# Kernel optimization log

Measured on AMD Instinct MI355X. Metric: run time of the kernel, lower is better.

## Reference

```python
import jax, jax.numpy as jnp
import numpy as np

H = 1024; B = 8; L = 4096
DI = 2048   # d_inner = expand*H
DS = 16     # d_state
DC = 4      # d_conv
DR = 64     # dt_rank = ceil(H/16)
HR = 256    # H // 4 hourglass


def setup_inputs() -> dict:
    key = jax.random.key(0)
    ks = jax.random.split(key, 16)
    w = lambda k, s, sc=0.02: jax.random.normal(k, s, jnp.float32) * sc
    return {
        "x": jax.random.normal(ks[0], (B, L, H), jnp.float32),
        "c": jax.random.normal(ks[1], (B, H), jnp.float32),
        "adaln_w": w(ks[2], (3 * H, H)), "adaln_b": jnp.zeros((3 * H,), jnp.float32),
        "hgd_w1": w(ks[3], (HR, H)), "hgd_b1": jnp.zeros((HR,), jnp.float32),
        "hgd_w2": w(ks[4], (H, HR)), "hgd_b2": jnp.zeros((H,), jnp.float32),
        "hgf_wm": w(ks[5], (HR, H)), "hgf_bm": jnp.zeros((HR,), jnp.float32),
        "hgf_wr": w(ks[6], (HR, H)), "hgf_br": jnp.zeros((HR,), jnp.float32),
        "hgf_wf": w(ks[7], (H, HR)), "hgf_bf": jnp.zeros((H,), jnp.float32),
        "in_w": w(ks[8], (2 * DI, H)),
        "conv_w": w(ks[9], (DI, DC), 0.1), "conv_b": jnp.zeros((DI,), jnp.float32),
        "xproj_w": w(ks[10], (DR + 2 * DS, DI)),
        "dtproj_w": w(ks[11], (DI, DR), 0.1),
        "dt_bias": jnp.full((DI,), -4.6, jnp.float32),  # softplus -> dt ~ 0.01
        "A_log": jnp.log(jnp.tile(jnp.arange(1, DS + 1, dtype=jnp.float32), (DI, 1))),
        "D": jnp.ones((DI,), jnp.float32),
        "out_w": w(ks[12], (H, DI)),
    }


def reference(x, c, adaln_w, adaln_b, hgd_w1, hgd_b1, hgd_w2, hgd_b2,
              hgf_wm, hgf_bm, hgf_wr, hgf_br, hgf_wf, hgf_bf,
              in_w, conv_w, conv_b, xproj_w, dtproj_w, dt_bias, A_log, D, out_w):
    silu = jax.nn.silu
    # adaLN-Zero conditioning: SiLU -> Linear -> 3 chunks
    mod = silu(c) @ adaln_w.T + adaln_b                      # [B, 3H]
    shift, scale, alpha = jnp.split(mod, 3, axis=1)          # each [B, H]
    # LayerNorm (no affine, eps=1e-6)
    mu = x.mean(-1, keepdims=True)
    var = x.var(-1, keepdims=True)
    xn = (x - mu) / jnp.sqrt(var + 1e-6)
    x1 = xn * (1.0 + scale[:, None, :]) + shift[:, None, :]  # modulate
    # Hourglass dense: Linear(H->H/4) -> SiLU -> Linear(H/4->H)
    hd = silu(x1 @ hgd_w1.T + hgd_b1) @ hgd_w2.T + hgd_b2    # [B, L, H]
    # ---- Mamba ----
    xz = hd @ in_w.T                                         # [B, L, 2*DI]
    xm, z = jnp.split(xz, 2, axis=-1)
    # causal depthwise conv1d
    xc = jnp.transpose(xm, (0, 2, 1))                        # [B, DI, L]
    xc = jax.lax.conv_general_dilated(
        xc, conv_w[:, None, :], (1,), [(DC - 1, 0)],
        feature_group_count=DI, dimension_numbers=("NCH", "OIH", "NCH"))
    xc = silu(xc + conv_b[None, :, None])
    xc = jnp.transpose(xc, (0, 2, 1))                        # [B, L, DI]
    # input-dependent dt, B, C
    dbl = xc @ xproj_w.T                                     # [B, L, DR+2*DS]
    dt, Bm, Cm = jnp.split(dbl, [DR, DR + DS], axis=-1)
    dt = jax.nn.softplus(dt @ dtproj_w.T + dt_bias)          # [B, L, DI]
    A = -jnp.exp(A_log)                                      # [DI, DS]
    # selective scan: h_{t} = exp(dt*A)*h_{t-1} + dt*B_t*x_t ; y_t = <h_t, C_t>
    def step(h, inp):
        dt_t, B_t, C_t, x_t = inp                            # [B,DI],[B,DS],[B,DS],[B,DI]
        h = h * jnp.exp(dt_t[:, :, None] * A) + (dt_t * x_t)[:, :, None] * B_t[:, None, :]
        return h, jnp.einsum("bds,bs->bd", h, C_t)
    h0 = jnp.zeros((x.shape[0], DI, DS), x.dtype)
    seq = (jnp.transpose(dt, (1, 0, 2)), jnp.transpose(Bm, (1, 0, 2)),
           jnp.transpose(Cm, (1, 0, 2)), jnp.transpose(xc, (1, 0, 2)))
    _, ys = jax.lax.scan(step, h0, seq)                      # [L, B, DI]
    y = jnp.transpose(ys, (1, 0, 2)) + xc * D
    y = y * silu(z)
    x1_2 = y @ out_w.T                                       # [B, L, H]
    # Hourglass fusion
    fused = (silu(x1_2 @ hgf_wm.T + hgf_bm) * silu(x1 @ hgf_wr.T + hgf_br)) @ hgf_wf.T + hgf_bf
    return x + alpha[:, None, :] * fused
```

## Files before the change

kernel.cpp:

```cpp
#include <hip/hip_runtime.h>

#define Hn 1024
#define Bn 8
#define Ln 4096
#define DIn 2048
#define NCH 64
#define CLn 64

typedef __attribute__((ext_vector_type(8))) short short8;
typedef __attribute__((ext_vector_type(4))) short short4v;
typedef __attribute__((ext_vector_type(4))) float f32x4;

__device__ __forceinline__ float bf2f(short s) {
  return __uint_as_float(((unsigned)(unsigned short)s) << 16);
}
__device__ __forceinline__ short f2bf(float f) {
  unsigned u = __float_as_uint(f);
  u += 0x7fffu + ((u >> 16) & 1u);
  return (short)(u >> 16);
}
__device__ __forceinline__ float silu_f(float x) { return x / (1.f + __expf(-x)); }
__device__ __forceinline__ float softplus_f(float x) { return x > 20.f ? x : log1pf(__expf(x)); }

__device__ __forceinline__ void gld16(const short* g, short* l) {
  __builtin_amdgcn_global_load_lds((const __attribute__((address_space(1))) void*)g,
                                   (__attribute__((address_space(3))) void*)l, 16, 0, 0);
}

__global__ __launch_bounds__(256) void f2bf4_kernel(const float* __restrict__ in,
                                                    short* __restrict__ out, int n4) {
  int i = blockIdx.x * 256 + threadIdx.x;
  if (i < n4) {
    f32x4 v = ((const f32x4*)in)[i];
    short4v o;
    o.x = f2bf(v.x); o.y = f2bf(v.y); o.z = f2bf(v.z); o.w = f2bf(v.w);
    ((short4v*)out)[i] = o;
  }
}

__global__ __launch_bounds__(256) void modcalc_kernel(const float* __restrict__ c,
    const float* __restrict__ aw, const float* __restrict__ ab, float* __restrict__ mod) {
  int wid = blockIdx.x * 4 + (threadIdx.x >> 6);
  int lane = threadIdx.x & 63;
  int b = wid / 3072, n = wid - b * 3072;
  const f32x4* cr = (const f32x4*)(c + b * Hn);
  const f32x4* wr = (const f32x4*)(aw + (size_t)n * Hn);
  float s = 0.f;
#pragma unroll
  for (int i = 0; i < 4; ++i) {
    f32x4 cv = cr[lane + 64 * i];
    f32x4 wv = wr[lane + 64 * i];
    s += silu_f(cv.x) * wv.x + silu_f(cv.y) * wv.y + silu_f(cv.z) * wv.z + silu_f(cv.w) * wv.w;
  }
#pragma unroll
  for (int m = 1; m < 64; m <<= 1) s += __shfl_xor(s, m, 64);
  if (lane == 0) mod[wid] = s + ab[n];
}

__global__ __launch_bounds__(256) void ln_mod_kernel(const float* __restrict__ x,
    const float* __restrict__ mod, short* __restrict__ x1, int b0) {
  int row = blockIdx.x * 4 + (threadIdx.x >> 6);
  int lane = threadIdx.x & 63;
  int b = b0 + (row >> 12);
  const f32x4* xr = (const f32x4*)(x + (size_t)row * Hn);
  f32x4 v[4];
  float s = 0.f, ss = 0.f;
#pragma unroll
  for (int i = 0; i < 4; ++i) {
    v[i] = xr[lane + 64 * i];
    s += v[i].x + v[i].y + v[i].z + v[i].w;
    ss += v[i].x * v[i].x + v[i].y * v[i].y + v[i].z * v[i].z + v[i].w * v[i].w;
  }
#pragma unroll
  for (int m = 1; m < 64; m <<= 1) {
    s += __shfl_xor(s, m, 64);
    ss += __shfl_xor(ss, m, 64);
  }
  float mu = s * (1.f / 1024.f);
  float var = ss * (1.f / 1024.f) - mu * mu;
  float r = rsqrtf(var + 1e-6f);
  const f32x4* shp = (const f32x4*)(mod + b * 3072);
  const f32x4* scp = (const f32x4*)(mod + b * 3072 + 1024);
#pragma unroll
  for (int i = 0; i < 4; ++i) {
    int k4 = lane + 64 * i;
    f32x4 sc = scp[k4], sh = shp[k4];
    short4v o;
    o.x = f2bf((v[i].x - mu) * r * (1.f + sc.x) + sh.x);
    o.y = f2bf((v[i].y - mu) * r * (1.f + sc.y) + sh.y);
    o.z = f2bf((v[i].z - mu) * r * (1.f + sc.z) + sh.z);
    o.w = f2bf((v[i].w - mu) * r * (1.f + sc.w) + sh.w);
    *(short4v*)&x1[(size_t)row * Hn + k4 * 4] = o;
  }
}

#define SA_STR 40
template <int EPI>
__global__ __launch_bounds__(256) void gemm_k(
    const short* __restrict__ A, const short* __restrict__ W,
    const float* __restrict__ bias, const short* mul,
    const float* __restrict__ xres, const float* __restrict__ modp,
    void* outp, int N, int K, int b0) {
  __shared__ short sA[2][128 * SA_STR];
  __shared__ short sB[2][128 * SA_STR];
  int tid = threadIdx.x;
  int wave = tid >> 6, lane = tid & 63;
  int bm0 = blockIdx.y * 128;
  int bn0 = blockIdx.x * 128;
  int wm = (wave >> 1) * 64, wn = (wave & 1) * 64;
  int lrow = lane & 15, kh = (lane >> 4) * 8;
  int srow = tid >> 2;
  int scol = (tid & 3) * 8;

  f32x4 acc[4][4];
#pragma unroll
  for (int i = 0; i < 4; i++)
#pragma unroll
    for (int j = 0; j < 4; j++) acc[i][j] = (f32x4)0.f;

#pragma unroll
  for (int p = 0; p < 2; ++p) {
    int r = srow + p * 64;
    short8 av = *(const short8*)&A[(size_t)(bm0 + r) * K + scol];
    *(short8*)&sA[0][r * SA_STR + scol] = av;
    int n = bn0 + r;
    short8 bv = (short8)0;
    if (n < N) bv = *(const short8*)&W[(size_t)n * K + scol];
    *(short8*)&sB[0][r * SA_STR + scol] = bv;
  }
  __syncthreads();

  int cur = 0;
  for (int k0 = 0; k0 < K; k0 += 32) {
    bool have = (k0 + 32) < K;
    short8 av[2], bv[2];
    if (have) {
#pragma unroll
      for (int p = 0; p < 2; ++p) {
        int r = srow + p * 64;
        av[p] = *(const short8*)&A[(size_t)(bm0 + r) * K + k0 + 32 + scol];
        int n = bn0 + r;
        bv[p] = (short8)0;
        if (n < N) bv[p] = *(const short8*)&W[(size_t)n * K + k0 + 32 + scol];
      }
    }
    short8 af[4], bfr[4];
#pragma unroll
    for (int i = 0; i < 4; i++) af[i] = *(const short8*)&sA[cur][(wm + i * 16 + lrow) * SA_STR + kh];
#pragma unroll
    for (int j = 0; j < 4; j++) bfr[j] = *(const short8*)&sB[cur][(wn + j * 16 + lrow) * SA_STR + kh];
#pragma unroll
    for (int i = 0; i < 4; i++)
#pragma unroll
      for (int j = 0; j < 4; j++)
        acc[i][j] = __builtin_amdgcn_mfma_f32_16x16x32_bf16(af[i], bfr[j], acc[i][j], 0, 0, 0);
    if (have) {
      int nxt = cur ^ 1;
#pragma unroll
      for (int p = 0; p < 2; ++p) {
        int r = srow + p * 64;
        *(short8*)&sA[nxt][r * SA_STR + scol] = av[p];
        *(short8*)&sB[nxt][r * SA_STR + scol] = bv[p];
      }
    }
    __syncthreads();
    cur ^= 1;
  }

  int orow4 = (lane >> 4) * 4;
  int ocol = lane & 15;
#pragma unroll
  for (int i = 0; i < 4; i++)
#pragma unroll
    for (int j = 0; j < 4; j++)
#pragma unroll
      for (int r = 0; r < 4; r++) {
        int row = bm0 + wm + i * 16 + orow4 + r;
        int col = bn0 + wn + j * 16 + ocol;
        if (col >= N) continue;
        float v = acc[i][j][r];
        size_t idx = (size_t)row * N + col;
        if (EPI == 0) {
          ((short*)outp)[idx] = f2bf(v);
        } else if (EPI == 1) {
          ((short*)outp)[idx] = f2bf(v + bias[col]);
        } else if (EPI == 2) {
          ((short*)outp)[idx] = f2bf(silu_f(v + bias[col]));
        } else if (EPI == 3) {
          ((short*)outp)[idx] = f2bf(softplus_f(v + bias[col]));
        } else if (EPI == 4) {
          float t = silu_f(v + bias[col]) * bf2f(mul[idx]);
          ((short*)outp)[idx] = f2bf(t);
        } else if (EPI == 5) {
          ((float*)outp)[idx] = v;
        } else if (EPI == 6) {
          int b = b0 + (row >> 12);
          float t = v + bias[col];
          ((float*)outp)[idx] = xres[idx] + modp[b * 3072 + 2048 + col] * t;
        } else if (EPI == 7) {
          float t = silu_f(v) * bf2f(mul[idx]);
          ((short*)outp)[idx] = f2bf(t);
        } else if (EPI == 8) {
          ((float*)outp)[idx] = v;
          if (col < 64) ((short*)mul)[(size_t)row * 64 + col] = f2bf(v);
        }
      }
}

template <int EPI>
__global__ __launch_bounds__(512, 1) void gemm256_k(
    const short* __restrict__ A, const short* __restrict__ W,
    const short* mul, void* outp, int N, int K) {
  __shared__ short sA[2][256 * 64];
  __shared__ short sB[2][256 * 64];
  int tid = threadIdx.x;
  int wave = tid >> 6, lane = tid & 63;
  int nwg = gridDim.x * gridDim.y;
  int orig = blockIdx.y * gridDim.x + blockIdx.x;
  int cpx = nwg >> 3;
  int wg = (orig & 7) * cpx + (orig >> 3);
  int bm0 = (wg / gridDim.x) * 256;
  int bn0 = (wg % gridDim.x) * 256;
  int wm = (wave >> 2) * 128, wn = (wave & 3) * 64;
  int lrow = lane & 15;
  int kq = (lane >> 4) * 8;
  int srow = tid >> 3;
  int scol = (tid & 7) * 8;
  int soff = srow * 64 + scol;

  const short* Ab = A + (size_t)(bm0 + srow) * K + scol;
  const short* Bb = W + (size_t)(bn0 + srow) * K + scol;

  f32x4 acc[8][4];
#pragma unroll
  for (int m = 0; m < 8; m++)
#pragma unroll
    for (int n = 0; n < 4; n++) acc[m][n] = (f32x4)0.f;

#pragma unroll
  for (int p = 0; p < 4; ++p) {
    gld16(Ab + (size_t)(64 * p) * K, &sA[0][soff + p * 64 * 64]);
    gld16(Bb + (size_t)(64 * p) * K, &sB[0][soff + p * 64 * 64]);
  }
  __syncthreads();

  int cur = 0;
  for (int k0 = 0; k0 < K; k0 += 64) {
    int nxt = cur ^ 1;
    if (k0 + 64 < K) {
#pragma unroll
      for (int p = 0; p < 4; ++p) {
        gld16(Ab + k0 + 64 + (size_t)(64 * p) * K, &sA[nxt][soff + p * 64 * 64]);
        gld16(Bb + k0 + 64 + (size_t)(64 * p) * K, &sB[nxt][soff + p * 64 * 64]);
      }
    }
#pragma unroll
    for (int ks = 0; ks < 2; ++ks) {
      short8 af[8], bfr[4];
#pragma unroll
      for (int m = 0; m < 8; ++m)
        af[m] = *(const short8*)&sA[cur][(wm + m * 16 + lrow) * 64 + ks * 32 + kq];
#pragma unroll
      for (int n = 0; n < 4; ++n)
        bfr[n] = *(const short8*)&sB[cur][(wn + n * 16 + lrow) * 64 + ks * 32 + kq];
#pragma unroll
      for (int m = 0; m < 8; ++m)
#pragma unroll
        for (int n = 0; n < 4; ++n)
          acc[m][n] = __builtin_amdgcn_mfma_f32_16x16x32_bf16(af[m], bfr[n], acc[m][n], 0, 0, 0);
    }
    __syncthreads();
    cur = nxt;
  }

  int orow4 = (lane >> 4) * 4;
  int ocol = lane & 15;
#pragma unroll
  for (int m = 0; m < 8; m++)
#pragma unroll
    for (int n = 0; n < 4; n++)
#pragma unroll
      for (int r = 0; r < 4; r++) {
        int row = bm0 + wm + m * 16 + orow4 + r;
        int col = bn0 + wn + n * 16 + ocol;
        float v = acc[m][n][r];
        size_t idx = (size_t)row * N + col;
        if (EPI == 0) {
          ((short*)outp)[idx] = f2bf(v);
        } else if (EPI == 7) {
          float t = silu_f(v) * bf2f(mul[idx]);
          ((short*)outp)[idx] = f2bf(t);
        }
      }
}

__global__ __launch_bounds__(256) void conv_kernel(const short* __restrict__ xm,
    const float* __restrict__ cw, const float* __restrict__ cb, short* __restrict__ xc) {
  size_t idx = (size_t)blockIdx.x * 256 + threadIdx.x;
  int d = (int)(idx & (DIn - 1));
  size_t bt = idx >> 11;
  int t = (int)(bt & (Ln - 1));
  f32x4 w = *(const f32x4*)(cw + d * 4);
  float wj[4] = {w.x, w.y, w.z, w.w};
  float acc = cb[d];
#pragma unroll
  for (int j = 0; j < 4; ++j) {
    int tt = t - 3 + j;
    if (tt >= 0) acc += bf2f(xm[(bt - 3 + j) * DIn + d]) * wj[j];
  }
  xc[idx] = f2bf(silu_f(acc));
}

__global__ __launch_bounds__(256) void scan_part1(const short* __restrict__ dt,
    const short* __restrict__ xc, const float* __restrict__ dbl,
    const float* __restrict__ A_log, float* __restrict__ hq, float* __restrict__ sd) {
  __shared__ float sB[CLn * 16];
  int tid = threadIdx.x;
  int g = blockIdx.x * 256 + tid;
  int d = g & (DIn - 1);
  int r = g >> 11;
  int c = r & (NCH - 1);
  int b = r >> 6;
  size_t rb = (size_t)b * Ln + (size_t)c * CLn;
  {
    int row = tid >> 2, q = tid & 3;
    *(f32x4*)&sB[row * 16 + q * 4] = *(const f32x4*)(dbl + (rb + row) * 96 + 64 + q * 4);
  }
  __syncthreads();
  float A[16], h[16];
#pragma unroll
  for (int s = 0; s < 16; ++s) {
    A[s] = -__expf(A_log[d * 16 + s]);
    h[s] = 0.f;
  }
  bool st = true;
#pragma unroll
  for (int s = 1; s < 16; ++s)
    st = st && (fabsf(A[s] - (float)(s + 1) * A[0]) <= 1e-4f * fabsf(A[s]));
  float A0 = A[0];
  float sum = 0.f;
  const short* dp = dt + rb * DIn + d;
  const short* xp = xc + rb * DIn + d;
  short dtn = *dp, xcn = *xp;
  if (st) {
    for (int t = 0; t < CLn; ++t) {
      float dtv = bf2f(dtn), xv = bf2f(xcn);
      int tn = (t + 1 < CLn) ? t + 1 : t;
      dtn = dp[(size_t)tn * DIn];
      xcn = xp[(size_t)tn * DIn];
      float u = dtv * xv;
      sum += dtv;
      const f32x4* bp = (const f32x4*)&sB[t * 16];
      f32x4 b0 = bp[0], b1 = bp[1], b2 = bp[2], b3 = bp[3];
      float bv[16] = {b0.x, b0.y, b0.z, b0.w, b1.x, b1.y, b1.z, b1.w,
                      b2.x, b2.y, b2.z, b2.w, b3.x, b3.y, b3.z, b3.w};
      float qe = __expf(dtv * A0);
      float pk = qe;
#pragma unroll
      for (int s = 0; s < 16; ++s) {
        h[s] = h[s] * pk + u * bv[s];
        pk *= qe;
      }
    }
  } else {
    for (int t = 0; t < CLn; ++t) {
      float dtv = bf2f(dtn), xv = bf2f(xcn);
      int tn = (t + 1 < CLn) ? t + 1 : t;
      dtn = dp[(size_t)tn * DIn];
      xcn = xp[(size_t)tn * DIn];
      float u = dtv * xv;
      sum += dtv;
      const f32x4* bp = (const f32x4*)&sB[t * 16];
      f32x4 b0 = bp[0], b1 = bp[1], b2 = bp[2], b3 = bp[3];
      float bv[16] = {b0.x, b0.y, b0.z, b0.w, b1.x, b1.y, b1.z, b1.w,
                      b2.x, b2.y, b2.z, b2.w, b3.x, b3.y, b3.z, b3.w};
#pragma unroll
      for (int s = 0; s < 16; ++s) h[s] = h[s] * __expf(dtv * A[s]) + u * bv[s];
    }
  }
  size_t bd = (size_t)b * DIn + d;
  f32x4* out = (f32x4*)(hq + (bd * NCH + c) * 16);
#pragma unroll
  for (int i = 0; i < 4; ++i) {
    f32x4 o; o.x = h[4 * i]; o.y = h[4 * i + 1]; o.z = h[4 * i + 2]; o.w = h[4 * i + 3];
    out[i] = o;
  }
  sd[bd * NCH + c] = sum;
}

__global__ __launch_bounds__(256) void scan_combine(const float* __restrict__ A_log,
    const float* __restrict__ sd, float* hq) {
  int g = blockIdx.x * 256 + threadIdx.x;
  int s = g & 15;
  size_t bd = (size_t)(g >> 4);
  int d = (int)(bd & (DIn - 1));
  float A = -__expf(A_log[d * 16 + s]);
  float H = 0.f;
  for (int c = 0; c < NCH; ++c) {
    size_t idx = (bd * NCH + c) * 16 + s;
    float he = hq[idx];
    float e = __expf(A * sd[bd * NCH + c]);
    hq[idx] = H;
    H = H * e + he;
  }
}

__global__ __launch_bounds__(256) void scan_part2(const short* dt,
    const short* __restrict__ xc, const float* __restrict__ dbl,
    const float* __restrict__ A_log, const float* __restrict__ Dv,
    const float* __restrict__ hq, short* y) {
  __shared__ float sBC[CLn * 32];
  int tid = threadIdx.x;
  int g = blockIdx.x * 256 + tid;
  int d = g & (DIn - 1);
  int r = g >> 11;
  int c = r & (NCH - 1);
  int b = r >> 6;
  size_t rb = (size_t)b * Ln + (size_t)c * CLn;
  {
    int row = tid >> 2, q = tid & 3;
    const float* src = dbl + (rb + row) * 96 + 64 + q * 8;
    *(f32x4*)&sBC[row * 32 + q * 8] = *(const f32x4*)src;
    *(f32x4*)&sBC[row * 32 + q * 8 + 4] = *(const f32x4*)(src + 4);
  }
  __syncthreads();
  size_t bd = (size_t)b * DIn + d;
  float A[16], h[16];
#pragma unroll
  for (int s = 0; s < 16; ++s) A[s] = -__expf(A_log[d * 16 + s]);
  const f32x4* hin = (const f32x4*)(hq + (bd * NCH + c) * 16);
#pragma unroll
  for (int i = 0; i < 4; ++i) {
    f32x4 qv = hin[i];
    h[4 * i] = qv.x; h[4 * i + 1] = qv.y; h[4 * i + 2] = qv.z; h[4 * i + 3] = qv.w;
  }
  bool st = true;
#pragma unroll
  for (int s = 1; s < 16; ++s)
    st = st && (fabsf(A[s] - (float)(s + 1) * A[0]) <= 1e-4f * fabsf(A[s]));
  float A0 = A[0];
  float Dd = Dv[d];
  const short* dp = dt + rb * DIn + d;
  const short* xp = xc + rb * DIn + d;
  short* yp = y + rb * DIn + d;
  short dtn = *dp, xcn = *xp;
  if (st) {
    for (int t = 0; t < CLn; ++t) {
      float dtv = bf2f(dtn), xv = bf2f(xcn);
      int tn = (t + 1 < CLn) ? t + 1 : t;
      dtn = dp[(size_t)tn * DIn];
      xcn = xp[(size_t)tn * DIn];
      float u = dtv * xv;
      const f32x4* pp = (const f32x4*)&sBC[t * 32];
      f32x4 v0 = pp[0], v1 = pp[1], v2 = pp[2], v3 = pp[3];
      f32x4 v4 = pp[4], v5 = pp[5], v6 = pp[6], v7 = pp[7];
      float bc[32] = {v0.x, v0.y, v0.z, v0.w, v1.x, v1.y, v1.z, v1.w,
                      v2.x, v2.y, v2.z, v2.w, v3.x, v3.y, v3.z, v3.w,
                      v4.x, v4.y, v4.z, v4.w, v5.x, v5.y, v5.z, v5.w,
                      v6.x, v6.y, v6.z, v6.w, v7.x, v7.y, v7.z, v7.w};
      float qe = __expf(dtv * A0);
      float pk = qe, acc = 0.f;
#pragma unroll
      for (int s = 0; s < 16; ++s) {
        h[s] = h[s] * pk + u * bc[s];
        acc += h[s] * bc[16 + s];
        pk *= qe;
      }
      yp[(size_t)t * DIn] = f2bf(acc + xv * Dd);
    }
  } else {
    for (int t = 0; t < CLn; ++t) {
      float dtv = bf2f(dtn), xv = bf2f(xcn);
      int tn = (t + 1 < CLn) ? t + 1 : t;
      dtn = dp[(size_t)tn * DIn];
      xcn = xp[(size_t)tn * DIn];
      float u = dtv * xv;
      const f32x4* pp = (const f32x4*)&sBC[t * 32];
      f32x4 v0 = pp[0], v1 = pp[1], v2 = pp[2], v3 = pp[3];
      f32x4 v4 = pp[4], v5 = pp[5], v6 = pp[6], v7 = pp[7];
      float bc[32] = {v0.x, v0.y, v0.z, v0.w, v1.x, v1.y, v1.z, v1.w,
                      v2.x, v2.y, v2.z, v2.w, v3.x, v3.y, v3.z, v3.w,
                      v4.x, v4.y, v4.z, v4.w, v5.x, v5.y, v5.z, v5.w,
                      v6.x, v6.y, v6.z, v6.w, v7.x, v7.y, v7.z, v7.w};
      float acc = 0.f;
#pragma unroll
      for (int s = 0; s < 16; ++s) {
        h[s] = h[s] * __expf(dtv * A[s]) + u * bc[s];
        acc += h[s] * bc[16 + s];
      }
      yp[(size_t)t * DIn] = f2bf(acc + xv * Dd);
    }
  }
}

extern "C" void kernel_launch(void* const* d_in, const int* in_sizes, int n_in,
                              void* d_out, int out_size, void* d_ws, size_t ws_size,
                              hipStream_t stream) {
  const float* x = (const float*)d_in[0];
  const float* c = (const float*)d_in[1];
  const float* adaln_w = (const float*)d_in[2];
  const float* adaln_b = (const float*)d_in[3];
  const float* hgd_w1 = (const float*)d_in[4];
  const float* hgd_b1 = (const float*)d_in[5];
  const float* hgd_w2 = (const float*)d_in[6];
  const float* hgd_b2 = (const float*)d_in[7];
  const float* hgf_wm = (const float*)d_in[8];
  const float* hgf_bm = (const float*)d_in[9];
  const float* hgf_wr = (const float*)d_in[10];
  const float* hgf_br = (const float*)d_in[11];
  const float* hgf_wf = (const float*)d_in[12];
  const float* hgf_bf = (const float*)d_in[13];
  const float* in_w = (const float*)d_in[14];
  const float* conv_w = (const float*)d_in[15];
  const float* conv_b = (const float*)d_in[16];
  const float* xproj_w = (const float*)d_in[17];
  const float* dtproj_w = (const float*)d_in[18];
  const float* dt_bias = (const float*)d_in[19];
  const float* A_log = (const float*)d_in[20];
  const float* Dv = (const float*)d_in[21];
  const float* out_w = (const float*)d_in[22];
  (void)in_sizes; (void)n_in; (void)out_size;

  char* ws = (char*)d_ws;
  size_t off = 0;
  auto alloc = [&](size_t bytes) -> void* {
    void* p = ws + off;
    off += (bytes + 255) & ~(size_t)255;
    return p;
  };
  short* w1b = (short*)alloc((size_t)256 * 1024 * 2);
  short* w2b = (short*)alloc((size_t)1024 * 256 * 2);
  short* wmb = (short*)alloc((size_t)256 * 1024 * 2);
  short* wrb = (short*)alloc((size_t)256 * 1024 * 2);
  short* wfb = (short*)alloc((size_t)1024 * 256 * 2);
  short* inwb = (short*)alloc((size_t)4096 * 1024 * 2);
  short* xpb = (short*)alloc((size_t)96 * 2048 * 2);
  short* dtpb = (short*)alloc((size_t)2048 * 64 * 2);
  short* owb = (short*)alloc((size_t)1024 * 2048 * 2);
  float* modb = (float*)alloc((size_t)Bn * 3072 * 4);
  size_t persist = off;

  int BC = 8;
  while (BC > 1 && persist + (size_t)BC * Ln * 14976 > ws_size) BC >>= 1;
  int nchunk = 8 / BC;
  size_t Mc = (size_t)BC * Ln;

  short* x1 = (short*)alloc(Mc * 1024 * 2);
  short* hd = (short*)alloc(Mc * 1024 * 2);
  short* xm = (short*)alloc(Mc * 2048 * 2);
  short* xct = (short*)alloc(Mc * 2048 * 2);
  float* dbl = (float*)alloc(Mc * 96 * 4);
  short* dtb = (short*)alloc(Mc * 64 * 2);
  float* hq = (float*)alloc((size_t)BC * DIn * NCH * 16 * 4);
  float* sd = (float*)alloc((size_t)BC * DIn * NCH * 4);
  short* t1 = xct;

  auto conv1 = [&](const float* src, short* dst, int n) {
    f2bf4_kernel<<<(n / 4 + 255) / 256, 256, 0, stream>>>(src, dst, n / 4);
  };
  conv1(hgd_w1, w1b, 256 * 1024);
  conv1(hgd_w2, w2b, 1024 * 256);
  conv1(hgf_wm, wmb, 256 * 1024);
  conv1(hgf_wr, wrb, 256 * 1024);
  conv1(hgf_wf, wfb, 1024 * 256);
  conv1(in_w, inwb, 4096 * 1024);
  conv1(xproj_w, xpb, 96 * 2048);
  conv1(dtproj_w, dtpb, 2048 * 64);
  conv1(out_w, owb, 1024 * 2048);

  modcalc_kernel<<<(Bn * 3072) / 4, 256, 0, stream>>>(c, adaln_w, adaln_b, modb);

  dim3 blk(256);
  dim3 blk512(512);
  int gy = (int)(Mc / 128);
  int gy256 = (int)(Mc / 256);
  for (int ck = 0; ck < nchunk; ++ck) {
    int b0 = ck * BC;
    const float* xch = x + (size_t)b0 * Ln * Hn;
    float* och = (float*)d_out + (size_t)b0 * Ln * Hn;

    ln_mod_kernel<<<(int)(Mc / 4), blk, 0, stream>>>(xch, modb, x1, b0);
    gemm_k<2><<<dim3(2, gy), blk, 0, stream>>>(x1, w1b, hgd_b1, nullptr, nullptr, nullptr, t1, 256, 1024, 0);
    gemm_k<1><<<dim3(8, gy), blk, 0, stream>>>(t1, w2b, hgd_b2, nullptr, nullptr, nullptr, hd, 1024, 256, 0);
    gemm256_k<0><<<dim3(8, gy256), blk512, 0, stream>>>(hd, inwb, nullptr, xm, 2048, 1024);
    conv_kernel<<<(int)(Mc * 2048 / 256), blk, 0, stream>>>(xm, conv_w, conv_b, xct);
    gemm_k<8><<<dim3(1, gy), blk, 0, stream>>>(xct, xpb, nullptr, dtb, nullptr, nullptr, dbl, 96, 2048, 0);
    gemm_k<3><<<dim3(16, gy), blk, 0, stream>>>(dtb, dtpb, dt_bias, nullptr, nullptr, nullptr, xm, 2048, 64, 0);
    scan_part1<<<(int)(BC * 512), blk, 0, stream>>>(xm, xct, dbl, A_log, hq, sd);
    scan_combine<<<(int)(BC * 128), blk, 0, stream>>>(A_log, sd, hq);
    scan_part2<<<(int)(BC * 512), blk, 0, stream>>>(xm, xct, dbl, A_log, Dv, hq, xm);
    gemm256_k<7><<<dim3(8, gy256), blk512, 0, stream>>>(hd, inwb + (size_t)2048 * 1024, xm, xm, 2048, 1024);
    gemm256_k<0><<<dim3(4, gy256), blk512, 0, stream>>>(xm, owb, nullptr, hd, 1024, 2048);
    gemm_k<2><<<dim3(2, gy), blk, 0, stream>>>(hd, wmb, hgf_bm, nullptr, nullptr, nullptr, t1, 256, 1024, 0);
    gemm_k<4><<<dim3(2, gy), blk, 0, stream>>>(x1, wrb, hgf_br, t1, nullptr, nullptr, t1, 256, 1024, 0);
    gemm_k<6><<<dim3(8, gy), blk, 0, stream>>>(t1, wfb, hgf_bf, nullptr, xch, modb, och, 1024, 256, b0);
  }
}
```

Measured before the change: 2.091 ms.

## Rewrite 256x256 GEMM as 8-phase pipelined kernel with swizzled LDS

Replaces the simple double-buffered 256x256 bf16 GEMM with an 8-phase schedule. Each K-tile pair is split into quarter MFMA blocks, and half-tile global-to-LDS loads are interleaved between them, separated by explicit barriers and sched_barrier fences. LDS uses an XOR-swizzled layout to avoid bank conflicts, and MFMA blocks run at raised wave priority. The aim is to hide global load latency and LDS read stalls behind matrix math, at the cost of many more barriers and hand-tuned vmcnt waits that depend on K being a multiple of 128.

Measured after the change: 2.102 ms. No clear change (+0.5%).

```diff
diff --git a/kernel.cpp b/kernel.cpp
--- a/kernel.cpp
+++ b/kernel.cpp
@@ -26,6 +26,14 @@
   __builtin_amdgcn_global_load_lds((const __attribute__((address_space(1))) void*)g,
                                    (__attribute__((address_space(3))) void*)l, 16, 0, 0);
 }
+
+#define PFENCE() __builtin_amdgcn_sched_barrier(0)
+#define PBAR()            \
+  do {                    \
+    PFENCE();             \
+    __builtin_amdgcn_s_barrier(); \
+    PFENCE();             \
+  } while (0)
 
 __global__ __launch_bounds__(256) void f2bf4_kernel(const float* __restrict__ in,
                                                     short* __restrict__ out, int n4) {
@@ -208,11 +216,11 @@
 }
 
 template <int EPI>
-__global__ __launch_bounds__(512, 1) void gemm256_k(
+__global__ __launch_bounds__(512, 1) void gemm256_8ph(
     const short* __restrict__ A, const short* __restrict__ W,
     const short* mul, void* outp, int N, int K) {
-  __shared__ short sA[2][256 * 64];
-  __shared__ short sB[2][256 * 64];
+  __shared__ short sMem[65536];
+  char* sRaw = (char*)sMem;
   int tid = threadIdx.x;
   int wave = tid >> 6, lane = tid & 63;
   int nwg = gridDim.x * gridDim.y;
@@ -221,58 +229,132 @@
   int wg = (orig & 7) * cpx + (orig >> 3);
   int bm0 = (wg / gridDim.x) * 256;
   int bn0 = (wg % gridDim.x) * 256;
+  int lrow = lane & 15;
+  int lnOff = lrow * 64 + (((lane >> 4) * 16) ^ ((lrow >> 3) << 5));
+  int aBase = (wave >> 2) * 16384 + lnOff;
+  int bBase = 32768 + ((wave & 3) >> 1) * 16384 + lnOff;
+  int bSub = (wave & 1) * 4;
+
+  int rS[2], cS[2], lSlot[2];
+#pragma unroll
+  for (int p = 0; p < 2; ++p) {
+    int s = p * 8 + wave;
+    rS[p] = (s >> 1) * 16 + (lane >> 2);
+    cS[p] = (s & 1) * 4 + ((lane & 3) ^ (((lane >> 5) & 1) << 1));
+    lSlot[p] = s * 1024 + lane * 16;
+  }
+
+  f32x4 acc[8][4];
+#pragma unroll
+  for (int m = 0; m < 8; m++)
+#pragma unroll
+    for (int n = 0; n < 4; n++) acc[m][n] = (f32x4)0.f;
+
+  auto stage = [&](const short* Mb, int row0, int tt, int hh, int isB) {
+    int rb = (tt & 1) * 65536 + isB * 32768 + hh * 16384;
+#pragma unroll
+    for (int p = 0; p < 2; ++p) {
+      const short* src = Mb + (size_t)(row0 + hh * 128 + rS[p]) * K + tt * 64 + cS[p] * 8;
+      gld16(src, (short*)(sRaw + rb + lSlot[p]));
+    }
+  };
+
+  short8 af[4][2], bfL[2][2], bfH[2][2];
+  auto loadA = [&](int mg, int bsel) {
+#pragma unroll
+    for (int m = 0; m < 4; ++m)
+#pragma unroll
+      for (int ks = 0; ks < 2; ++ks)
+        af[m][ks] =
+            *(const short8*)(sRaw + bsel * 65536 + aBase + ((mg * 4 + m) * 2 + ks) * 1024);
+  };
+  auto loadB = [&](short8(&bf)[2][2], int ng, int bsel) {
+#pragma unroll
+    for (int n = 0; n < 2; ++n)
+#pragma unroll
+      for (int ks = 0; ks < 2; ++ks)
+        bf[n][ks] = *(const short8*)(sRaw + bsel * 65536 + bBase +
+                                     ((bSub + ng * 2 + n) * 2 + ks) * 1024);
+  };
+  auto mmaQ = [&](short8(&bf)[2][2], int mg, int ng) {
+    __builtin_amdgcn_s_setprio(1);
+#pragma unroll
+    for (int ks = 0; ks < 2; ++ks)
+#pragma unroll
+      for (int m = 0; m < 4; ++m)
+#pragma unroll
+        for (int n = 0; n < 2; ++n)
+          acc[mg * 4 + m][ng * 2 + n] = __builtin_amdgcn_mfma_f32_16x16x32_bf16(
+              af[m][ks], bf[n][ks], acc[mg * 4 + m][ng * 2 + n], 0, 0, 0);
+    __builtin_amdgcn_s_setprio(0);
+  };
+
+  stage(A, bm0, 0, 0, 0);
+  stage(A, bm0, 0, 1, 0);
+  stage(W, bn0, 0, 0, 1);
+  stage(W, bn0, 0, 1, 1);
+  stage(W, bn0, 1, 0, 1);
+  stage(W, bn0, 1, 1, 1);
+  asm volatile("s_waitcnt vmcnt(4)" ::: "memory");
+  PBAR();
+
+  int NT = K >> 6;
+  for (int t = 0; t < NT; t += 2) {
+    int s2 = (t + 2) < NT, s3 = (t + 3) < NT;
+    loadA(0, 0);
+    loadB(bfL, 0, 0);
+    stage(A, bm0, t + 1, 0, 0);
+    PBAR();
+    mmaQ(bfL, 0, 0);
+    PBAR();
+    loadB(bfH, 1, 0);
+    stage(A, bm0, t + 1, 1, 0);
+    PBAR();
+    mmaQ(bfH, 0, 1);
+    PBAR();
+    loadA(1, 0);
+    if (s2) stage(W, bn0, t + 2, 0, 1);
+    PBAR();
+    mmaQ(bfL, 1, 0);
+    PBAR();
+    if (s2) {
+      stage(W, bn0, t + 2, 1, 1);
+      asm volatile("s_waitcnt vmcnt(4)" ::: "memory");
+    } else {
+      asm volatile("s_waitcnt vmcnt(0)" ::: "memory");
+    }
+    PBAR();
+    mmaQ(bfH, 1, 1);
+    PBAR();
+    loadA(0, 1);
+    loadB(bfL, 0, 1);
+    if (s2) stage(A, bm0, t + 2, 0, 0);
+    PBAR();
+    mmaQ(bfL, 0, 0);
+    PBAR();
+    loadB(bfH, 1, 1);
+    if (s2) stage(A, bm0, t + 2, 1, 0);
+    PBAR();
+    mmaQ(bfH, 0, 1);
+    PBAR();
+    loadA(1, 1);
+    if (s3) stage(W, bn0, t + 3, 0, 1);
+    PBAR();
+    mmaQ(bfL, 1, 0);
+    PBAR();
+    if (s3) stage(W, bn0, t + 3, 1, 1);
+    if (s2) {
+      if (s3)
+        asm volatile("s_waitcnt vmcnt(4)" ::: "memory");
+      else
+        asm volatile("s_waitcnt vmcnt(0)" ::: "memory");
+    }
+    PBAR();
+    mmaQ(bfH, 1, 1);
+    PBAR();
+  }
+
   int wm = (wave >> 2) * 128, wn = (wave & 3) * 64;
-  int lrow = lane & 15;
-  int kq = (lane >> 4) * 8;
-  int srow = tid >> 3;
-  int scol = (tid & 7) * 8;
-  int soff = srow * 64 + scol;
-
-  const short* Ab = A + (size_t)(bm0 + srow) * K + scol;
-  const short* Bb = W + (size_t)(bn0 + srow) * K + scol;
-
-  f32x4 acc[8][4];
-#pragma unroll
-  for (int m = 0; m < 8; m++)
-#pragma unroll
-    for (int n = 0; n < 4; n++) acc[m][n] = (f32x4)0.f;
-
-#pragma unroll
-  for (int p = 0; p < 4; ++p) {
-    gld16(Ab + (size_t)(64 * p) * K, &sA[0][soff + p * 64 * 64]);
-    gld16(Bb + (size_t)(64 * p) * K, &sB[0][soff + p * 64 * 64]);
-  }
-  __syncthreads();
-
-  int cur = 0;
-  for (int k0 = 0; k0 < K; k0 += 64) {
-    int nxt = cur ^ 1;
-    if (k0 + 64 < K) {
-#pragma unroll
-      for (int p = 0; p < 4; ++p) {
-        gld16(Ab + k0 + 64 + (size_t)(64 * p) * K, &sA[nxt][soff + p * 64 * 64]);
-        gld16(Bb + k0 + 64 + (size_t)(64 * p) * K, &sB[nxt][soff + p * 64 * 64]);
-      }
-    }
-#pragma unroll
-    for (int ks = 0; ks < 2; ++ks) {
-      short8 af[8], bfr[4];
-#pragma unroll
-      for (int m = 0; m < 8; ++m)
-        af[m] = *(const short8*)&sA[cur][(wm + m * 16 + lrow) * 64 + ks * 32 + kq];
-#pragma unroll
-      for (int n = 0; n < 4; ++n)
-        bfr[n] = *(const short8*)&sB[cur][(wn + n * 16 + lrow) * 64 + ks * 32 + kq];
-#pragma unroll
-      for (int m = 0; m < 8; ++m)
-#pragma unroll
-        for (int n = 0; n < 4; ++n)
-          acc[m][n] = __builtin_amdgcn_mfma_f32_16x16x32_bf16(af[m], bfr[n], acc[m][n], 0, 0, 0);
-    }
-    __syncthreads();
-    cur = nxt;
-  }
-
   int orow4 = (lane >> 4) * 4;
   int ocol = lane & 15;
 #pragma unroll
@@ -582,15 +664,15 @@
     ln_mod_kernel<<<(int)(Mc / 4), blk, 0, stream>>>(xch, modb, x1, b0);
     gemm_k<2><<<dim3(2, gy), blk, 0, stream>>>(x1, w1b, hgd_b1, nullptr, nullptr, nullptr, t1, 256, 1024, 0);
     gemm_k<1><<<dim3(8, gy), blk, 0, stream>>>(t1, w2b, hgd_b2, nullptr, nullptr, nullptr, hd, 1024, 256, 0);
-    gemm256_k<0><<<dim3(8, gy256), blk512, 0, stream>>>(hd, inwb, nullptr, xm, 2048, 1024);
+    gemm256_8ph<0><<<dim3(8, gy256), blk512, 0, stream>>>(hd, inwb, nullptr, xm, 2048, 1024);
     conv_kernel<<<(int)(Mc * 2048 / 256), blk, 0, stream>>>(xm, conv_w, conv_b, xct);
     gemm_k<8><<<dim3(1, gy), blk, 0, stream>>>(xct, xpb, nullptr, dtb, nullptr, nullptr, dbl, 96, 2048, 0);
     gemm_k<3><<<dim3(16, gy), blk, 0, stream>>>(dtb, dtpb, dt_bias, nullptr, nullptr, nullptr, xm, 2048, 64, 0);
     scan_part1<<<(int)(BC * 512), blk, 0, stream>>>(xm, xct, dbl, A_log, hq, sd);
     scan_combine<<<(int)(BC * 128), blk, 0, stream>>>(A_log, sd, hq);
     scan_part2<<<(int)(BC * 512), blk, 0, stream>>>(xm, xct, dbl, A_log, Dv, hq, xm);
-    gemm256_k<7><<<dim3(8, gy256), blk512, 0, stream>>>(hd, inwb + (size_t)2048 * 1024, xm, xm, 2048, 1024);
-    gemm256_k<0><<<dim3(4, gy256), blk512, 0, stream>>>(xm, owb, nullptr, hd, 1024, 2048);
+    gemm256_8ph<7><<<dim3(8, gy256), blk512, 0, stream>>>(hd, inwb + (size_t)2048 * 1024, xm, xm, 2048, 1024);
+    gemm256_8ph<0><<<dim3(4, gy256), blk512, 0, stream>>>(xm, owb, nullptr, hd, 1024, 2048);
     gemm_k<2><<<dim3(2, gy), blk, 0, stream>>>(hd, wmb, hgf_bm, nullptr, nullptr, nullptr, t1, 256, 1024, 0);
     gemm_k<4><<<dim3(2, gy), blk, 0, stream>>>(x1, wrb, hgf_br, t1, nullptr, nullptr, t1, 256, 1024, 0);
     gemm_k<6><<<dim3(8, gy), blk, 0, stream>>>(t1, wfb, hgf_bf, nullptr, xch, modb, och, 1024, 256, b0);
```
